# Optimization experiments

Hardware: AMD Instinct MI355X
Metric: run time of the kernel (lower is better)

Reference implementation:

```python
import jax, jax.numpy as jnp
import numpy as np

B, N, C = 4, 1024, 768          # batch, tokens, embed_dim
D, H, HD, FF = 12, 12, 64, 3072  # depth, heads, head_dim, mlp hidden
LN_EPS = 1e-5


def setup_inputs() -> dict:
    key = jax.random.key(0)
    ks = jax.random.split(key, 12)
    w = lambda i, shape: jax.random.normal(ks[i], shape, jnp.float32) * 0.02
    return {
        "x": jax.random.normal(ks[0], (B, N, C), jnp.float32),
        "pos_x": jax.random.normal(ks[1], (B, N, C), jnp.float32),
        # stacked per-layer params (leading dim D)
        "qkv_w": w(2, (D, 3 * C, C)), "qkv_b": w(3, (D, 3 * C)),
        "proj_w": w(4, (D, C, C)),    "proj_b": w(5, (D, C)),
        "fc1_w": w(6, (D, FF, C)),    "fc1_b": w(7, (D, FF)),
        "fc2_w": w(8, (D, C, FF)),    "fc2_b": w(9, (D, C)),
        "ln1_g": jnp.ones((D, C), jnp.float32), "ln1_b": jnp.zeros((D, C), jnp.float32),
        "ln2_g": jnp.ones((D, C), jnp.float32), "ln2_b": jnp.zeros((D, C), jnp.float32),
        "normf_g": jnp.ones((C,), jnp.float32), "normf_b": jnp.zeros((C,), jnp.float32),
    }


def _ln(x, g, b):
    mu = jnp.mean(x, axis=-1, keepdims=True)
    var = jnp.mean((x - mu) ** 2, axis=-1, keepdims=True)
    return (x - mu) * jax.lax.rsqrt(var + LN_EPS) * g + b


def reference(x, pos_x, qkv_w, qkv_b, proj_w, proj_b, fc1_w, fc1_b, fc2_w, fc2_b,
              ln1_g, ln1_b, ln2_g, ln2_b, normf_g, normf_b):
    scale = 1.0 / jnp.sqrt(jnp.float32(HD))
    x = x + pos_x  # pos added once (add_pos_at_every_layer=False)

    def block(xc, p):
        qw, qb, pw, pb, f1w, f1b, f2w, f2b, g1, b1, g2, b2 = p
        h = _ln(xc, g1, b1)
        qkv = jnp.einsum('bnc,oc->bno', h, qw) + qb            # [B,N,3C]
        qkv = qkv.reshape(B, N, 3, H, HD).transpose(2, 0, 3, 1, 4)
        q, k, v = qkv[0], qkv[1], qkv[2]                       # [B,H,N,HD]
        attn = jax.nn.softmax(jnp.einsum('bhnd,bhmd->bhnm', q, k) * scale, axis=-1)
        o = jnp.einsum('bhnm,bhmd->bhnd', attn, v)
        o = o.transpose(0, 2, 1, 3).reshape(B, N, C)
        xc = xc + (jnp.einsum('bnc,oc->bno', o, pw) + pb)      # residual + proj
        h2 = _ln(xc, g2, b2)
        hid = jax.nn.gelu(jnp.einsum('bnc,fc->bnf', h2, f1w) + f1b, approximate=False)
        ffn = jnp.einsum('bnf,of->bno', hid, f2w) + f2b
        xc = xc + ffn
        return xc, None

    xs = (qkv_w, qkv_b, proj_w, proj_b, fc1_w, fc1_b, fc2_w, fc2_b,
          ln1_g, ln1_b, ln2_g, ln2_b)
    x, _ = jax.lax.scan(block, x, xs)
    return _ln(x, normf_g, normf_b)  # postnorm
```

## Files before the change

kernel.cpp:

```cpp
#include <hip/hip_runtime.h>
#include <hip/hip_bf16.h>
#include <math.h>

typedef __bf16 bf16;
typedef __bf16 bf16x8 __attribute__((ext_vector_type(8)));
typedef __bf16 bf16x4 __attribute__((ext_vector_type(4)));
typedef float  f32x4  __attribute__((ext_vector_type(4)));

#define B_  4
#define N_  1024
#define C_  768
#define H_  12
#define HD_ 64
#define FF_ 3072
#define T_  (B_*N_)
#define D_  12

__device__ __forceinline__ void gld_lds16(const void* g, void* l) {
    __builtin_amdgcn_global_load_lds(
        (const __attribute__((address_space(1))) void*)g,
        (__attribute__((address_space(3))) void*)l, 16, 0, 0);
}

template<typename WT, int MODE>
__global__ __launch_bounds__(256) void gemm_bt(
    const bf16* __restrict__ A, const WT* __restrict__ Bt,
    const float* __restrict__ bias, bf16* __restrict__ out,
    float* __restrict__ resid, int M, int N, int Kfull, int Ks)
{
    __shared__ __align__(16) bf16 lA[128*32];
    __shared__ __align__(16) WT   lB[128*32];
    const int tid  = threadIdx.x;
    const int lane = tid & 63, wave = tid >> 6;
    const int lo = lane & 15, hi = lane >> 4;
    const int wm = wave & 1, wn = wave >> 1;
    const int row0 = blockIdx.x * 128, col0 = blockIdx.y * 128;
    const int k0base = blockIdx.z * Ks;

    f32x4 acc[4][4];
#pragma unroll
    for (int i = 0; i < 4; i++)
#pragma unroll
        for (int j = 0; j < 4; j++) acc[i][j] = (f32x4){0.f, 0.f, 0.f, 0.f};

    for (int k0 = k0base; k0 < k0base + Ks; k0 += 32) {
#pragma unroll
        for (int r = 0; r < 2; ++r) {
            const int cb    = r * 256 + wave * 64;
            const int chunk = cb + lane;
            const int rw = chunk >> 2, kc = chunk & 3;
            gld_lds16(A + (size_t)(row0 + rw) * Kfull + k0 + kc * 8, lA + cb * 8);
        }
        if constexpr (sizeof(WT) == 2) {
#pragma unroll
            for (int r = 0; r < 2; ++r) {
                const int cb    = r * 256 + wave * 64;
                const int chunk = cb + lane;
                const int rw = chunk >> 2, kc = chunk & 3;
                gld_lds16(Bt + (size_t)(col0 + rw) * Kfull + k0 + kc * 8,
                          (bf16*)lB + cb * 8);
            }
        } else {
#pragma unroll
            for (int r = 0; r < 4; ++r) {
                const int cb    = r * 256 + wave * 64;
                const int chunk = cb + lane;
                const int rw = chunk >> 3, kc = chunk & 7;
                const int kcs = kc ^ (rw & 7);
                gld_lds16(Bt + (size_t)(col0 + rw) * Kfull + k0 + kcs * 4,
                          (float*)lB + cb * 4);
            }
        }
        __syncthreads();
        bf16x8 af[4], bfr[4];
#pragma unroll
        for (int i = 0; i < 4; i++)
            af[i]  = *(const bf16x8*)(lA + (wm * 64 + i * 16 + lo) * 32 + hi * 8);
#pragma unroll
        for (int i = 0; i < 4; i++) {
            if constexpr (sizeof(WT) == 2) {
                bfr[i] = *(const bf16x8*)((const bf16*)lB +
                             (wn * 64 + i * 16 + lo) * 32 + hi * 8);
            } else {
                const float* base = (const float*)lB + (wn * 64 + i * 16 + lo) * 32;
                const int sw = lo & 7;
                const f32x4 u0 = *(const f32x4*)(base + (((hi * 2)     ^ sw) * 4));
                const f32x4 u1 = *(const f32x4*)(base + (((hi * 2 + 1) ^ sw) * 4));
                bf16x8 f;
#pragma unroll
                for (int e = 0; e < 4; e++) { f[e] = (bf16)u0[e]; f[4+e] = (bf16)u1[e]; }
                bfr[i] = f;
            }
        }
#pragma unroll
        for (int mi = 0; mi < 4; mi++)
#pragma unroll
            for (int ni = 0; ni < 4; ni++)
                acc[mi][ni] = __builtin_amdgcn_mfma_f32_16x16x32_bf16(
                    af[mi], bfr[ni], acc[mi][ni], 0, 0, 0);
        __syncthreads();
    }

    const float bscale = (blockIdx.z == 0) ? 1.0f : 0.0f;
#pragma unroll
    for (int mi = 0; mi < 4; mi++) {
#pragma unroll
        for (int ni = 0; ni < 4; ni++) {
            const int gcol = col0 + wn * 64 + ni * 16 + lo;
            const float bv = bias[gcol] * bscale;
#pragma unroll
            for (int r = 0; r < 4; r++) {
                const int grow = row0 + wm * 64 + mi * 16 + hi * 4 + r;
                float v = acc[mi][ni][r] + bv;
                if (MODE == 1) v = 0.5f * v * (1.0f + erff(v * 0.70710678118f));
                if (MODE == 2) {
                    atomicAdd(&resid[(size_t)grow * N + gcol], v);
                } else {
                    out[(size_t)grow * N + gcol] = (bf16)v;
                }
            }
        }
    }
}

__global__ __launch_bounds__(256) void cvt_k(
    const float* __restrict__ src, bf16* __restrict__ dst)
{
    const int i = (blockIdx.x * 256 + threadIdx.x) * 8;
    const f32x4 a = *(const f32x4*)(src + i);
    const f32x4 b = *(const f32x4*)(src + i + 4);
    bf16x8 o;
#pragma unroll
    for (int e = 0; e < 4; e++) { o[e] = (bf16)a[e]; o[4 + e] = (bf16)b[e]; }
    *(bf16x8*)(dst + i) = o;
}

template<typename OutT>
__global__ __launch_bounds__(256) void ln_k(
    const float* __restrict__ x, const float* __restrict__ g,
    const float* __restrict__ b, OutT* __restrict__ out)
{
    const int wave = threadIdx.x >> 6, lane = threadIdx.x & 63;
    const int t = blockIdx.x * 4 + wave;
    const float* row = x + (size_t)t * C_;
    f32x4 v[3];
    float s = 0.f, ss = 0.f;
#pragma unroll
    for (int j = 0; j < 3; j++) {
        v[j] = *(const f32x4*)(row + (j * 64 + lane) * 4);
#pragma unroll
        for (int e = 0; e < 4; e++) { s += v[j][e]; ss += v[j][e] * v[j][e]; }
    }
#pragma unroll
    for (int off = 32; off > 0; off >>= 1) {
        s  += __shfl_xor(s, off);
        ss += __shfl_xor(ss, off);
    }
    const float mu  = s * (1.f / 768.f);
    const float var = ss * (1.f / 768.f) - mu * mu;
    const float rs  = rsqrtf(var + 1e-5f);
    OutT* orow = out + (size_t)t * C_;
#pragma unroll
    for (int j = 0; j < 3; j++) {
        const f32x4 gv = *(const f32x4*)(g + (j * 64 + lane) * 4);
        const f32x4 bv = *(const f32x4*)(b + (j * 64 + lane) * 4);
#pragma unroll
        for (int e = 0; e < 4; e++)
            orow[(j * 64 + lane) * 4 + e] = (OutT)((v[j][e] - mu) * rs * gv[e] + bv[e]);
    }
}

__global__ __launch_bounds__(256) void addpos_k(
    const float* __restrict__ x, const float* __restrict__ p, float* __restrict__ o)
{
    const int i = (blockIdx.x * 256 + threadIdx.x) * 4;
    const f32x4 xv = *(const f32x4*)(x + i);
    const f32x4 pv = *(const f32x4*)(p + i);
    f32x4 ov;
#pragma unroll
    for (int e = 0; e < 4; e++) ov[e] = xv[e] + pv[e];
    *(f32x4*)(o + i) = ov;
}

#define SK_ 72
__global__ __launch_bounds__(256) void attn_k(
    const bf16* __restrict__ qkv, bf16* __restrict__ out)
{
    const int qt = blockIdx.x;
    const int bh = blockIdx.y;
    const int b = bh / H_, h = bh % H_;
    const int lane = threadIdx.x & 63, wave = threadIdx.x >> 6;
    const int lo = lane & 15, hi = lane >> 4;

    __shared__ __align__(16) bf16 lK[64 * SK_];
    __shared__ __align__(16) bf16 lV[64 * SK_];
    __shared__ __align__(16) bf16 lP[4][16 * SK_];

    const size_t tokbase = (size_t)b * N_;

    const bf16* qptr = qkv + (tokbase + qt * 64 + wave * 16 + lo) * (3 * C_) + h * HD_;
    const bf16x8 qf0 = *(const bf16x8*)(qptr + hi * 8);
    const bf16x8 qf1 = *(const bf16x8*)(qptr + 32 + hi * 8);

    float m_r[4], l_r[4];
    f32x4 oacc[4];
#pragma unroll
    for (int r = 0; r < 4; r++) { m_r[r] = -1e30f; l_r[r] = 0.f; }
#pragma unroll
    for (int di = 0; di < 4; di++) oacc[di] = (f32x4){0.f, 0.f, 0.f, 0.f};

    for (int kt = 0; kt < 16; ++kt) {
        const int kb0 = kt * 64;
#pragma unroll
        for (int r = 0; r < 2; ++r) {
            const int chunk = r * 256 + threadIdx.x;
            const int key = chunk >> 3, dc = chunk & 7;
            const bf16* kp = qkv + (tokbase + kb0 + key) * (3 * C_) + C_ + h * HD_ + dc * 8;
            *(bf16x8*)(lK + key * SK_ + dc * 8) = *(const bf16x8*)kp;
        }
#pragma unroll
        for (int r = 0; r < 2; ++r) {
            const int chunk = r * 256 + threadIdx.x;
            const int d = chunk & 63, kg = chunk >> 6;
            const bf16* vp = qkv + (tokbase + kb0 + kg * 8) * (3 * C_)
                           + 2 * C_ + h * HD_ + d;
            bf16x8 tv;
#pragma unroll
            for (int i = 0; i < 8; i++) tv[i] = vp[(size_t)i * (3 * C_)];
            *(bf16x8*)(lV + d * SK_ + kg * 8) = tv;
        }
        __syncthreads();

        f32x4 sacc[4];
#pragma unroll
        for (int kb = 0; kb < 4; kb++) {
            const bf16x8 b0 = *(const bf16x8*)(lK + (kb * 16 + lo) * SK_ + hi * 8);
            const bf16x8 b1 = *(const bf16x8*)(lK + (kb * 16 + lo) * SK_ + 32 + hi * 8);
            f32x4 a = (f32x4){0.f, 0.f, 0.f, 0.f};
            a = __builtin_amdgcn_mfma_f32_16x16x32_bf16(qf0, b0, a, 0, 0, 0);
            a = __builtin_amdgcn_mfma_f32_16x16x32_bf16(qf1, b1, a, 0, 0, 0);
            sacc[kb] = a;
        }

        float tm[4], mn[4], alpha[4], ts[4], ps[4][4];
#pragma unroll
        for (int r = 0; r < 4; r++) {
            tm[r] = fmaxf(fmaxf(sacc[0][r], sacc[1][r]),
                          fmaxf(sacc[2][r], sacc[3][r])) * 0.125f;
#pragma unroll
            for (int off = 1; off < 16; off <<= 1)
                tm[r] = fmaxf(tm[r], __shfl_xor(tm[r], off));
            mn[r] = fmaxf(m_r[r], tm[r]);
            alpha[r] = __expf(m_r[r] - mn[r]);
            ts[r] = 0.f;
        }
#pragma unroll
        for (int kb = 0; kb < 4; kb++)
#pragma unroll
            for (int r = 0; r < 4; r++) {
                const float p = __expf(sacc[kb][r] * 0.125f - mn[r]);
                ps[kb][r] = p;
                ts[r] += p;
            }
#pragma unroll
        for (int r = 0; r < 4; r++) {
#pragma unroll
            for (int off = 1; off < 16; off <<= 1)
                ts[r] += __shfl_xor(ts[r], off);
            l_r[r] = l_r[r] * alpha[r] + ts[r];
            m_r[r] = mn[r];
        }
#pragma unroll
        for (int di = 0; di < 4; di++)
#pragma unroll
            for (int r = 0; r < 4; r++) oacc[di][r] *= alpha[r];

#pragma unroll
        for (int kb = 0; kb < 4; kb++)
#pragma unroll
            for (int r = 0; r < 4; r++)
                lP[wave][(hi * 4 + r) * SK_ + kb * 16 + lo] = (bf16)ps[kb][r];

        const bf16x8 pa0 = *(const bf16x8*)(&lP[wave][lo * SK_ + hi * 8]);
        const bf16x8 pa1 = *(const bf16x8*)(&lP[wave][lo * SK_ + 32 + hi * 8]);
#pragma unroll
        for (int di = 0; di < 4; di++) {
            const bf16x8 v0 = *(const bf16x8*)(lV + (di * 16 + lo) * SK_ + hi * 8);
            const bf16x8 v1 = *(const bf16x8*)(lV + (di * 16 + lo) * SK_ + 32 + hi * 8);
            oacc[di] = __builtin_amdgcn_mfma_f32_16x16x32_bf16(pa0, v0, oacc[di], 0, 0, 0);
            oacc[di] = __builtin_amdgcn_mfma_f32_16x16x32_bf16(pa1, v1, oacc[di], 0, 0, 0);
        }
        __syncthreads();
    }

#pragma unroll
    for (int di = 0; di < 4; di++)
#pragma unroll
        for (int r = 0; r < 4; r++) {
            const size_t tok = tokbase + qt * 64 + wave * 16 + hi * 4 + r;
            out[tok * C_ + h * HD_ + di * 16 + lo] = (bf16)(oacc[di][r] / l_r[r]);
        }
}

extern "C" void kernel_launch(void* const* d_in, const int* in_sizes, int n_in,
                              void* d_out, int out_size, void* d_ws, size_t ws_size,
                              hipStream_t stream)
{
    const float* x      = (const float*)d_in[0];
    const float* pos_x  = (const float*)d_in[1];
    const float* qkv_w  = (const float*)d_in[2];
    const float* qkv_b  = (const float*)d_in[3];
    const float* proj_w = (const float*)d_in[4];
    const float* proj_b = (const float*)d_in[5];
    const float* fc1_w  = (const float*)d_in[6];
    const float* fc1_b  = (const float*)d_in[7];
    const float* fc2_w  = (const float*)d_in[8];
    const float* fc2_b  = (const float*)d_in[9];
    const float* ln1_g  = (const float*)d_in[10];
    const float* ln1_b  = (const float*)d_in[11];
    const float* ln2_g  = (const float*)d_in[12];
    const float* ln2_b  = (const float*)d_in[13];
    const float* nf_g   = (const float*)d_in[14];
    const float* nf_b   = (const float*)d_in[15];

    char* ws = (char*)d_ws;
    float* xres  = (float*)(ws);
    bf16* hbuf   = (bf16*)(ws + 12582912);
    bf16* qkvbuf = (bf16*)(ws + 18874368);
    bf16* attno  = (bf16*)(ws + 37748736);
    bf16* hid    = (bf16*)(ws + 44040192);
    bf16* wq     = (bf16*)(ws + 69206016);
    bf16* wp     = (bf16*)(ws + 111673344);
    bf16* w1     = (bf16*)(ws + 125829120);
    bf16* w2     = (bf16*)(ws + 182452224);
    const bool usebf16 = ws_size >= (size_t)239075328;

    addpos_k<<<T_ * C_ / 4 / 256, 256, 0, stream>>>(x, pos_x, xres);

    if (usebf16) {
        cvt_k<<<D_ * 3 * C_ * C_ / 2048, 256, 0, stream>>>(qkv_w, wq);
        cvt_k<<<D_ * C_ * C_ / 2048, 256, 0, stream>>>(proj_w, wp);
        cvt_k<<<D_ * FF_ * C_ / 2048, 256, 0, stream>>>(fc1_w, w1);
        cvt_k<<<D_ * C_ * FF_ / 2048, 256, 0, stream>>>(fc2_w, w2);
    }

    for (int L = 0; L < D_; ++L) {
        ln_k<bf16><<<T_ / 4, 256, 0, stream>>>(xres, ln1_g + L * C_, ln1_b + L * C_, hbuf);
        if (usebf16) {
            gemm_bt<bf16,0><<<dim3(T_/128, (3*C_)/128, 1), 256, 0, stream>>>(
                hbuf, wq + (size_t)L * 3 * C_ * C_, qkv_b + (size_t)L * 3 * C_,
                qkvbuf, nullptr, T_, 3 * C_, C_, C_);
        } else {
            gemm_bt<float,0><<<dim3(T_/128, (3*C_)/128, 1), 256, 0, stream>>>(
                hbuf, qkv_w + (size_t)L * 3 * C_ * C_, qkv_b + (size_t)L * 3 * C_,
                qkvbuf, nullptr, T_, 3 * C_, C_, C_);
        }
        attn_k<<<dim3(N_ / 64, B_ * H_), 256, 0, stream>>>(qkvbuf, attno);
        if (usebf16) {
            gemm_bt<bf16,2><<<dim3(T_/128, C_/128, 2), 256, 0, stream>>>(
                attno, wp + (size_t)L * C_ * C_, proj_b + (size_t)L * C_,
                nullptr, xres, T_, C_, C_, C_ / 2);
        } else {
            gemm_bt<float,2><<<dim3(T_/128, C_/128, 2), 256, 0, stream>>>(
                attno, proj_w + (size_t)L * C_ * C_, proj_b + (size_t)L * C_,
                nullptr, xres, T_, C_, C_, C_ / 2);
        }
        ln_k<bf16><<<T_ / 4, 256, 0, stream>>>(xres, ln2_g + L * C_, ln2_b + L * C_, hbuf);
        if (usebf16) {
            gemm_bt<bf16,1><<<dim3(T_/128, FF_/128, 1), 256, 0, stream>>>(
                hbuf, w1 + (size_t)L * FF_ * C_, fc1_b + (size_t)L * FF_,
                hid, nullptr, T_, FF_, C_, C_);
            gemm_bt<bf16,2><<<dim3(T_/128, C_/128, 2), 256, 0, stream>>>(
                hid, w2 + (size_t)L * C_ * FF_, fc2_b + (size_t)L * C_,
                nullptr, xres, T_, C_, FF_, FF_ / 2);
        } else {
            gemm_bt<float,1><<<dim3(T_/128, FF_/128, 1), 256, 0, stream>>>(
                hbuf, fc1_w + (size_t)L * FF_ * C_, fc1_b + (size_t)L * FF_,
                hid, nullptr, T_, FF_, C_, C_);
            gemm_bt<float,2><<<dim3(T_/128, C_/128, 2), 256, 0, stream>>>(
                hid, fc2_w + (size_t)L * C_ * FF_, fc2_b + (size_t)L * C_,
                nullptr, xres, T_, C_, FF_, FF_ / 2);
        }
    }
    ln_k<float><<<T_ / 4, 256, 0, stream>>>(xres, nf_g, nf_b, (float*)d_out);
}
```

Measured before the change: 2.943 ms.

## Deepen GEMM K-tile to 64 with XOR swizzle and widen attention key tiles

```diff
diff --git a/kernel.cpp b/kernel.cpp
--- a/kernel.cpp
+++ b/kernel.cpp
@@ -28,8 +28,8 @@
     const float* __restrict__ bias, bf16* __restrict__ out,
     float* __restrict__ resid, int M, int N, int Kfull, int Ks)
 {
-    __shared__ __align__(16) bf16 lA[128*32];
-    __shared__ __align__(16) WT   lB[128*32];
+    __shared__ __align__(16) bf16 lA[128*64];
+    __shared__ __align__(16) WT   lB[128*64];
     const int tid  = threadIdx.x;
     const int lane = tid & 63, wave = tid >> 6;
     const int lo = lane & 15, hi = lane >> 4;
@@ -43,61 +43,70 @@
 #pragma unroll
         for (int j = 0; j < 4; j++) acc[i][j] = (f32x4){0.f, 0.f, 0.f, 0.f};
 
-    for (int k0 = k0base; k0 < k0base + Ks; k0 += 32) {
-#pragma unroll
-        for (int r = 0; r < 2; ++r) {
+    for (int k0 = k0base; k0 < k0base + Ks; k0 += 64) {
+#pragma unroll
+        for (int r = 0; r < 4; ++r) {
             const int cb    = r * 256 + wave * 64;
             const int chunk = cb + lane;
-            const int rw = chunk >> 2, kc = chunk & 3;
-            gld_lds16(A + (size_t)(row0 + rw) * Kfull + k0 + kc * 8, lA + cb * 8);
+            const int rw = chunk >> 3, kc = chunk & 7;
+            const int kcs = kc ^ (rw & 7);
+            gld_lds16(A + (size_t)(row0 + rw) * Kfull + k0 + kcs * 8, lA + cb * 8);
         }
         if constexpr (sizeof(WT) == 2) {
-#pragma unroll
-            for (int r = 0; r < 2; ++r) {
-                const int cb    = r * 256 + wave * 64;
-                const int chunk = cb + lane;
-                const int rw = chunk >> 2, kc = chunk & 3;
-                gld_lds16(Bt + (size_t)(col0 + rw) * Kfull + k0 + kc * 8,
-                          (bf16*)lB + cb * 8);
-            }
-        } else {
 #pragma unroll
             for (int r = 0; r < 4; ++r) {
                 const int cb    = r * 256 + wave * 64;
                 const int chunk = cb + lane;
                 const int rw = chunk >> 3, kc = chunk & 7;
                 const int kcs = kc ^ (rw & 7);
+                gld_lds16(Bt + (size_t)(col0 + rw) * Kfull + k0 + kcs * 8,
+                          (bf16*)lB + cb * 8);
+            }
+        } else {
+#pragma unroll
+            for (int r = 0; r < 8; ++r) {
+                const int cb    = r * 256 + wave * 64;
+                const int chunk = cb + lane;
+                const int rw = chunk >> 4, kc = chunk & 15;
+                const int kcs = kc ^ ((rw & 7) << 1);
                 gld_lds16(Bt + (size_t)(col0 + rw) * Kfull + k0 + kcs * 4,
                           (float*)lB + cb * 4);
             }
         }
         __syncthreads();
-        bf16x8 af[4], bfr[4];
-#pragma unroll
-        for (int i = 0; i < 4; i++)
-            af[i]  = *(const bf16x8*)(lA + (wm * 64 + i * 16 + lo) * 32 + hi * 8);
-#pragma unroll
-        for (int i = 0; i < 4; i++) {
-            if constexpr (sizeof(WT) == 2) {
-                bfr[i] = *(const bf16x8*)((const bf16*)lB +
-                             (wn * 64 + i * 16 + lo) * 32 + hi * 8);
-            } else {
-                const float* base = (const float*)lB + (wn * 64 + i * 16 + lo) * 32;
-                const int sw = lo & 7;
-                const f32x4 u0 = *(const f32x4*)(base + (((hi * 2)     ^ sw) * 4));
-                const f32x4 u1 = *(const f32x4*)(base + (((hi * 2 + 1) ^ sw) * 4));
-                bf16x8 f;
-#pragma unroll
-                for (int e = 0; e < 4; e++) { f[e] = (bf16)u0[e]; f[4+e] = (bf16)u1[e]; }
-                bfr[i] = f;
-            }
-        }
-#pragma unroll
-        for (int mi = 0; mi < 4; mi++)
-#pragma unroll
-            for (int ni = 0; ni < 4; ni++)
-                acc[mi][ni] = __builtin_amdgcn_mfma_f32_16x16x32_bf16(
-                    af[mi], bfr[ni], acc[mi][ni], 0, 0, 0);
+#pragma unroll 1
+        for (int s = 0; s < 2; ++s) {
+            bf16x8 af[4], bfr[4];
+#pragma unroll
+            for (int i = 0; i < 4; i++) {
+                const int rowA = wm * 64 + i * 16 + lo;
+                const int ca = (s * 4 + hi) ^ (lo & 7);
+                af[i] = *(const bf16x8*)(lA + rowA * 64 + ca * 8);
+            }
+#pragma unroll
+            for (int i = 0; i < 4; i++) {
+                const int rowB = wn * 64 + i * 16 + lo;
+                if constexpr (sizeof(WT) == 2) {
+                    const int cb = (s * 4 + hi) ^ (lo & 7);
+                    bfr[i] = *(const bf16x8*)((const bf16*)lB + rowB * 64 + cb * 8);
+                } else {
+                    const float* base = (const float*)lB + rowB * 64;
+                    const int c0 = (s * 8 + hi * 2) ^ ((lo & 7) << 1);
+                    const f32x4 u0 = *(const f32x4*)(base + c0 * 4);
+                    const f32x4 u1 = *(const f32x4*)(base + (c0 + 1) * 4);
+                    bf16x8 f;
+#pragma unroll
+                    for (int e = 0; e < 4; e++) { f[e] = (bf16)u0[e]; f[4+e] = (bf16)u1[e]; }
+                    bfr[i] = f;
+                }
+            }
+#pragma unroll
+            for (int mi = 0; mi < 4; mi++)
+#pragma unroll
+                for (int ni = 0; ni < 4; ni++)
+                    acc[mi][ni] = __builtin_amdgcn_mfma_f32_16x16x32_bf16(
+                        af[mi], bfr[ni], acc[mi][ni], 0, 0, 0);
+        }
         __syncthreads();
     }
 
@@ -182,7 +191,9 @@
     *(f32x4*)(o + i) = ov;
 }
 
-#define SK_ 72
+#define SKD_ 72
+#define SVK_ 136
+#define SPK_ 136
 __global__ __launch_bounds__(256) void attn_k(
     const bf16* __restrict__ qkv, bf16* __restrict__ out)
 {
@@ -192,15 +203,20 @@
     const int lane = threadIdx.x & 63, wave = threadIdx.x >> 6;
     const int lo = lane & 15, hi = lane >> 4;
 
-    __shared__ __align__(16) bf16 lK[64 * SK_];
-    __shared__ __align__(16) bf16 lV[64 * SK_];
-    __shared__ __align__(16) bf16 lP[4][16 * SK_];
+    __shared__ __align__(16) bf16 lK[128 * SKD_];
+    __shared__ __align__(16) bf16 lV[64 * SVK_];
+    __shared__ __align__(16) bf16 lP[4][16 * SPK_];
 
     const size_t tokbase = (size_t)b * N_;
 
     const bf16* qptr = qkv + (tokbase + qt * 64 + wave * 16 + lo) * (3 * C_) + h * HD_;
-    const bf16x8 qf0 = *(const bf16x8*)(qptr + hi * 8);
-    const bf16x8 qf1 = *(const bf16x8*)(qptr + 32 + hi * 8);
+    bf16x8 qf0 = *(const bf16x8*)(qptr + hi * 8);
+    bf16x8 qf1 = *(const bf16x8*)(qptr + 32 + hi * 8);
+#pragma unroll
+    for (int e = 0; e < 8; e++) {
+        qf0[e] = (bf16)((float)qf0[e] * 0.125f);
+        qf1[e] = (bf16)((float)qf1[e] * 0.125f);
+    }
 
     float m_r[4], l_r[4];
     f32x4 oacc[4];
@@ -209,17 +225,17 @@
 #pragma unroll
     for (int di = 0; di < 4; di++) oacc[di] = (f32x4){0.f, 0.f, 0.f, 0.f};
 
-    for (int kt = 0; kt < 16; ++kt) {
-        const int kb0 = kt * 64;
-#pragma unroll
-        for (int r = 0; r < 2; ++r) {
+    for (int kt = 0; kt < 8; ++kt) {
+        const int kb0 = kt * 128;
+#pragma unroll
+        for (int r = 0; r < 4; ++r) {
             const int chunk = r * 256 + threadIdx.x;
             const int key = chunk >> 3, dc = chunk & 7;
             const bf16* kp = qkv + (tokbase + kb0 + key) * (3 * C_) + C_ + h * HD_ + dc * 8;
-            *(bf16x8*)(lK + key * SK_ + dc * 8) = *(const bf16x8*)kp;
-        }
-#pragma unroll
-        for (int r = 0; r < 2; ++r) {
+            *(bf16x8*)(lK + key * SKD_ + dc * 8) = *(const bf16x8*)kp;
+        }
+#pragma unroll
+        for (int r = 0; r < 4; ++r) {
             const int chunk = r * 256 + threadIdx.x;
             const int d = chunk & 63, kg = chunk >> 6;
             const bf16* vp = qkv + (tokbase + kb0 + kg * 8) * (3 * C_)
@@ -227,26 +243,29 @@
             bf16x8 tv;
 #pragma unroll
             for (int i = 0; i < 8; i++) tv[i] = vp[(size_t)i * (3 * C_)];
-            *(bf16x8*)(lV + d * SK_ + kg * 8) = tv;
+            *(bf16x8*)(lV + d * SVK_ + kg * 8) = tv;
         }
         __syncthreads();
 
-        f32x4 sacc[4];
-#pragma unroll
-        for (int kb = 0; kb < 4; kb++) {
-            const bf16x8 b0 = *(const bf16x8*)(lK + (kb * 16 + lo) * SK_ + hi * 8);
-            const bf16x8 b1 = *(const bf16x8*)(lK + (kb * 16 + lo) * SK_ + 32 + hi * 8);
+        f32x4 sacc[8];
+#pragma unroll
+        for (int kb = 0; kb < 8; kb++) {
+            const bf16x8 b0 = *(const bf16x8*)(lK + (kb * 16 + lo) * SKD_ + hi * 8);
+            const bf16x8 b1 = *(const bf16x8*)(lK + (kb * 16 + lo) * SKD_ + 32 + hi * 8);
             f32x4 a = (f32x4){0.f, 0.f, 0.f, 0.f};
             a = __builtin_amdgcn_mfma_f32_16x16x32_bf16(qf0, b0, a, 0, 0, 0);
             a = __builtin_amdgcn_mfma_f32_16x16x32_bf16(qf1, b1, a, 0, 0, 0);
             sacc[kb] = a;
         }
 
-        float tm[4], mn[4], alpha[4], ts[4], ps[4][4];
+        float tm[4], mn[4], alpha[4], ts[4];
 #pragma unroll
         for (int r = 0; r < 4; r++) {
-            tm[r] = fmaxf(fmaxf(sacc[0][r], sacc[1][r]),
-                          fmaxf(sacc[2][r], sacc[3][r])) * 0.125f;
+            float a0 = fmaxf(fmaxf(sacc[0][r], sacc[1][r]),
+                             fmaxf(sacc[2][r], sacc[3][r]));
+            float a1 = fmaxf(fmaxf(sacc[4][r], sacc[5][r]),
+                             fmaxf(sacc[6][r], sacc[7][r]));
+            tm[r] = fmaxf(a0, a1);
 #pragma unroll
             for (int off = 1; off < 16; off <<= 1)
                 tm[r] = fmaxf(tm[r], __shfl_xor(tm[r], off));
@@ -255,11 +274,11 @@
             ts[r] = 0.f;
         }
 #pragma unroll
-        for (int kb = 0; kb < 4; kb++)
+        for (int kb = 0; kb < 8; kb++)
 #pragma unroll
             for (int r = 0; r < 4; r++) {
-                const float p = __expf(sacc[kb][r] * 0.125f - mn[r]);
-                ps[kb][r] = p;
+                const float p = __expf(sacc[kb][r] - mn[r]);
+                lP[wave][(hi * 4 + r) * SPK_ + kb * 16 + lo] = (bf16)p;
                 ts[r] += p;
             }
 #pragma unroll
@@ -275,20 +294,17 @@
 #pragma unroll
             for (int r = 0; r < 4; r++) oacc[di][r] *= alpha[r];
 
-#pragma unroll
-        for (int kb = 0; kb < 4; kb++)
-#pragma unroll
-            for (int r = 0; r < 4; r++)
-                lP[wave][(hi * 4 + r) * SK_ + kb * 16 + lo] = (bf16)ps[kb][r];
-
-        const bf16x8 pa0 = *(const bf16x8*)(&lP[wave][lo * SK_ + hi * 8]);
-        const bf16x8 pa1 = *(const bf16x8*)(&lP[wave][lo * SK_ + 32 + hi * 8]);
+        bf16x8 pa[4];
+#pragma unroll
+        for (int s = 0; s < 4; s++)
+            pa[s] = *(const bf16x8*)(&lP[wave][lo * SPK_ + s * 32 + hi * 8]);
 #pragma unroll
         for (int di = 0; di < 4; di++) {
-            const bf16x8 v0 = *(const bf16x8*)(lV + (di * 16 + lo) * SK_ + hi * 8);
-            const bf16x8 v1 = *(const bf16x8*)(lV + (di * 16 + lo) * SK_ + 32 + hi * 8);
-            oacc[di] = __builtin_amdgcn_mfma_f32_16x16x32_bf16(pa0, v0, oacc[di], 0, 0, 0);
-            oacc[di] = __builtin_amdgcn_mfma_f32_16x16x32_bf16(pa1, v1, oacc[di], 0, 0, 0);
+#pragma unroll
+            for (int s = 0; s < 4; s++) {
+                const bf16x8 v = *(const bf16x8*)(lV + (di * 16 + lo) * SVK_ + s * 32 + hi * 8);
+                oacc[di] = __builtin_amdgcn_mfma_f32_16x16x32_bf16(pa[s], v, oacc[di], 0, 0, 0);
+            }
         }
         __syncthreads();
     }
```

Result: faster. 2.647 ms (-10.1%).
